# Performance work log

Hardware: AMD Instinct MI355X
Metric: run time of the kernel (lower is better)

The kernel has to match this reference:

```python
import jax, jax.numpy as jnp
import numpy as np

TAU = 1.0
TOP_P = 0.9
EPS = 1e-5


def _nucleus_adj(X, W1, W2, W3):
    h = jnp.tanh(X @ W1.T)            # [N, d_attn]
    q = h @ W2.T                      # [N, d_attn]
    k = X @ W3.T                      # [N, d_attn]
    scores = (q @ k.T) / TAU          # [N, N]
    probs = jax.nn.softmax(scores, axis=-1)
    # nucleus (top-p): keep smallest prefix of desc-sorted probs covering mass p
    order = jnp.argsort(-probs, axis=-1)
    sp = jnp.take_along_axis(probs, order, axis=-1)
    cs = jnp.cumsum(sp, axis=-1)
    keep_sorted = (cs - sp) < TOP_P   # keep tokens before mass exceeds p (incl. crossing one)
    inv = jnp.argsort(order, axis=-1)
    keep = jnp.take_along_axis(keep_sorted, inv, axis=-1)
    A = jnp.where(keep, probs, 0.0)
    return A / jnp.sum(A, axis=-1, keepdims=True)


def _sequence_priors(N, dtype):
    # forward/backward chain priors (S=None case): row-stochastic shift matrices
    Rf = jnp.eye(N, k=-1, dtype=dtype).at[0, 0].set(1.0)
    Rb = jnp.eye(N, k=1, dtype=dtype).at[N - 1, N - 1].set(1.0)
    return Rf, Rb


def setup_inputs() -> dict:
    key = jax.random.key(0)
    ks = jax.random.split(key, 8)
    N, d_in, d_attn, steps = 4096, 512, 64, 2
    s = 0.02
    return {
        "X": jax.random.normal(ks[0], (N, d_in), jnp.float32),
        "W1": jax.random.normal(ks[1], (d_attn, d_in), jnp.float32) * s,
        "W2": jax.random.normal(ks[2], (d_attn, d_attn), jnp.float32) * s,
        "W3": jax.random.normal(ks[3], (d_attn, d_in), jnp.float32) * s,
        "U1": jax.random.normal(ks[4], (steps, d_in, d_in), jnp.float32) * s,
        "U2": jax.random.normal(ks[5], (steps, d_in, d_in), jnp.float32) * s,
        "U3": jax.random.normal(ks[6], (steps, d_in, d_in), jnp.float32) * s,
        "gamma": jnp.ones((d_in,), jnp.float32),
        "beta": jnp.zeros((d_in,), jnp.float32),
    }


def reference(X, W1, W2, W3, U1, U2, U3, gamma, beta):
    N = X.shape[0]
    steps = U1.shape[0]
    Rf, Rb = _sequence_priors(N, X.dtype)
    Z = jnp.zeros_like(X)
    Xf, Xb, Xa = X, X, X
    for n in range(steps):
        A = _nucleus_adj(Xa, W1, W2, W3)
        Xf = Rf @ Xf
        Xb = Rb @ Xb
        Xa = A @ Xa
        P = Xf @ U1[n].T + Xb @ U2[n].T
        F = Xa @ U3[n].T
        Z = Z + (P + F)  # dropout is identity in eval mode
    y = X + Z
    mu = jnp.mean(y, axis=-1, keepdims=True)
    var = jnp.var(y, axis=-1, keepdims=True)
    return (y - mu) * jax.lax.rsqrt(var + EPS) * gamma + beta
```

## Files before the change

kernel.cpp:

```cpp
#include <hip/hip_runtime.h>
#include <hip/hip_bf16.h>
#include <math.h>

typedef short bf16x8 __attribute__((ext_vector_type(8)));
typedef float f32x4 __attribute__((ext_vector_type(4)));
typedef unsigned short u16;
typedef unsigned long long u64;

#define N_TOK  4096
#define D_IN   512
#define D_ATTN 64
#define NBI    1024
#define CAPW   128
#define TOPP   0.9f
#define LN_EPS 1e-5f
#define AMAXV  (N_TOK - 1)
#define FLTMAX 3.402823466e38f
#define MSCALE 524288.0f

__device__ __forceinline__ u16 f2bf(float f) {
  unsigned int u = __float_as_uint(f);
  return (u16)((u + 0x7FFFu + ((u >> 16) & 1u)) >> 16);
}

__device__ __forceinline__ float bf2f(u16 v) {
  return __uint_as_float(((unsigned)v) << 16);
}

__device__ __forceinline__ unsigned mfix(float e) {
  return (unsigned)(e * MSCALE + 0.5f);
}

__device__ __forceinline__ void gload16(const u16* g, u16* l) {
  __builtin_amdgcn_global_load_lds(
      (const __attribute__((address_space(1))) unsigned int*)g,
      (__attribute__((address_space(3))) unsigned int*)l, 16, 0, 0);
}

template<int EPI, int NSEG, int KSEG>
__global__ __launch_bounds__(256)
void gemm128(const u16* __restrict__ A0, int lda0, int sh0, const u16* __restrict__ B0, int ldb0,
             const u16* __restrict__ A1, int lda1, int sh1, const u16* __restrict__ B1, int ldb1,
             const u16* __restrict__ A2, int lda2, int sh2, const u16* __restrict__ B2, int ldb2,
             float* __restrict__ Cf, u16* __restrict__ Cb, u16* __restrict__ CbT,
             int ldc, int ldct)
{
  constexpr int BN = 64;
  constexpr int NF = BN / 32;
  __shared__ u16 sA[3][128 * 64];
  __shared__ u16 sB[3][BN * 64];

  const int tid  = threadIdx.x;
  const int wave = tid >> 6;
  const int lane = tid & 63;
  const int l15  = lane & 15;
  const int l4   = lane >> 4;
  const int brow = blockIdx.y << 7;
  const int bcol = blockIdx.x * BN;
  const int kz   = blockIdx.z * KSEG;
  const int wr64 = (wave >> 1) << 6;
  const int wcol = (wave & 1) * (BN >> 1);

  constexpr int IPSEG = KSEG >> 6;
  constexpr int TOTAL = NSEG * IPSEG;

  auto stage = [&](int buf, int it) {
    int seg = (NSEG == 1) ? 0 : (it / IPSEG);
    int kk  = (NSEG == 1) ? (it << 6) : ((it % IPSEG) << 6);
    const u16 *Ab, *Bb; int la, lb, sh;
    if (seg == 0)      { Ab = A0; la = lda0; sh = sh0; Bb = B0; lb = ldb0; }
    else if (seg == 1) { Ab = A1; la = lda1; sh = sh1; Bb = B1; lb = ldb1; }
    else               { Ab = A2; la = lda2; sh = sh2; Bb = B2; lb = ldb2; }
    kk += kz;
#pragma unroll
    for (int q = 0; q < 4; ++q) {
      int idx = q * 256 + tid;
      int row = idx >> 3;
      int chunk = (idx & 7) ^ (row & 7);
      int r = brow + row + sh;
      r = (r < 0) ? 0 : ((r > AMAXV) ? AMAXV : r);
      gload16(Ab + (size_t)r * la + kk + chunk * 8, &sA[buf][idx * 8]);
    }
#pragma unroll
    for (int q = 0; q < BN / 32; ++q) {
      int idx = q * 256 + tid;
      int row = idx >> 3;
      int chunk = (idx & 7) ^ (row & 7);
      gload16(Bb + (size_t)(bcol + row) * lb + kk + chunk * 8, &sB[buf][idx * 8]);
    }
  };

  f32x4 acc[4][NF];
#pragma unroll
  for (int m = 0; m < 4; ++m)
#pragma unroll
    for (int n = 0; n < NF; ++n) {
      acc[m][n][0] = 0.f; acc[m][n][1] = 0.f; acc[m][n][2] = 0.f; acc[m][n][3] = 0.f;
    }

  stage(0, 0);
  if (TOTAL > 1) stage(1, 1);

  for (int i = 0; i < TOTAL; ++i) {
    if (i + 1 < TOTAL) asm volatile("s_waitcnt vmcnt(6)" ::: "memory");
    else               asm volatile("s_waitcnt vmcnt(0)" ::: "memory");
    __builtin_amdgcn_s_barrier();
    if (i + 2 < TOTAL) stage((i + 2) % 3, i + 2);
    const int c = i % 3;
#pragma unroll
    for (int ks = 0; ks < 2; ++ks) {
      bf16x8 af[4], bfr[NF];
#pragma unroll
      for (int m = 0; m < 4; ++m) {
        int ar = wr64 + m * 16 + l15;
        af[m] = *(const bf16x8*)&sA[c][ar * 64 + (((ks << 2) + l4) ^ (ar & 7)) * 8];
      }
#pragma unroll
      for (int n = 0; n < NF; ++n) {
        int br = wcol + n * 16 + l15;
        bfr[n] = *(const bf16x8*)&sB[c][br * 64 + (((ks << 2) + l4) ^ (br & 7)) * 8];
      }
#pragma unroll
      for (int m = 0; m < 4; ++m)
#pragma unroll
        for (int n = 0; n < NF; ++n)
          acc[m][n] = __builtin_amdgcn_mfma_f32_16x16x32_bf16(af[m], bfr[n], acc[m][n], 0, 0, 0);
    }
  }

  float* Cf6 = (EPI == 6) ? (Cf + (size_t)blockIdx.z * (size_t)ldct) : Cf;
#pragma unroll
  for (int m = 0; m < 4; ++m)
#pragma unroll
    for (int n = 0; n < NF; ++n)
#pragma unroll
      for (int r = 0; r < 4; ++r) {
        const int row = brow + wr64 + m * 16 + l4 * 4 + r;
        const int col = bcol + wcol + n * 16 + l15;
        const float v = acc[m][n][r];
        if (EPI == 0) Cf[(size_t)row * ldc + col] = v;
        if (EPI == 1) Cb[(size_t)row * ldc + col] = f2bf(tanhf(v));
        if (EPI == 2) Cb[(size_t)row * ldc + col] = f2bf(v);
        if (EPI == 3) Cf[(size_t)row * ldc + col] += v;
        if (EPI == 4) {
          u16 hv = f2bf(v);
          Cb [(size_t)row * ldc  + col] = hv;
          CbT[(size_t)col * ldct + row] = hv;
        }
        if (EPI == 5) {
          if (col < 64) Cb [(size_t)row * 64 + col]        = f2bf(tanhf(v));
          else          CbT[(size_t)row * 64 + (col - 64)] = f2bf(v);
        }
        if (EPI == 6) Cf6[(size_t)row * ldc + col] = v;
      }
}

__global__ __launch_bounds__(256)
void pvfix(const float* __restrict__ Zp, u16* __restrict__ Xa, u16* __restrict__ XaT)
{
  const size_t st = (size_t)N_TOK * D_IN;
  __shared__ u16 tile[64][65];
  const int bx = blockIdx.x, by = blockIdx.y;
  const int t = threadIdx.x;
  const int tx = t & 15, ty = t >> 4;
#pragma unroll
  for (int i = 0; i < 4; ++i) {
    int r = by * 64 + ty + 16 * i;
    int c = bx * 64 + tx * 4;
    size_t idx = (size_t)r * D_IN + c;
    float4 a = *(const float4*)&Zp[idx];
    float4 b = *(const float4*)&Zp[idx + st];
    float4 d = *(const float4*)&Zp[idx + 2 * st];
    float4 e = *(const float4*)&Zp[idx + 3 * st];
    u16 q0 = f2bf(a.x + b.x + d.x + e.x), q1 = f2bf(a.y + b.y + d.y + e.y);
    u16 q2 = f2bf(a.z + b.z + d.z + e.z), q3 = f2bf(a.w + b.w + d.w + e.w);
    *(ushort4*)&Xa[idx] = make_ushort4(q0, q1, q2, q3);
    tile[ty + 16 * i][tx * 4 + 0] = q0;
    tile[ty + 16 * i][tx * 4 + 1] = q1;
    tile[ty + 16 * i][tx * 4 + 2] = q2;
    tile[ty + 16 * i][tx * 4 + 3] = q3;
  }
  __syncthreads();
#pragma unroll
  for (int i = 0; i < 4; ++i) {
    int cc = ty + 16 * i;
    int rq = tx * 4;
    u16 o0 = tile[rq + 0][cc], o1 = tile[rq + 1][cc];
    u16 o2 = tile[rq + 2][cc], o3 = tile[rq + 3][cc];
    *(ushort4*)&XaT[(size_t)(bx * 64 + cc) * N_TOK + by * 64 + rq] =
        make_ushort4(o0, o1, o2, o3);
  }
}

__global__ __launch_bounds__(256, 8)
void nucleus_block(const u16* __restrict__ S, u16* __restrict__ A, int apitch)
{
  const int t = threadIdx.x;
  const int wv = t >> 6, ln = t & 63;

  __shared__ unsigned hist[4][NBI];
  __shared__ float ge[CAPW];
  __shared__ unsigned gm[CAPW];
  __shared__ int   gcol[CAPW];
  __shared__ unsigned char kf[CAPW];
  __shared__ float sMax[4], sMin[4];
  __shared__ int   sCnt[4];
  __shared__ unsigned sScan[4];
  __shared__ u64   sKey[4];
  __shared__ int   s_cnt;

  for (int rr = 0; rr < 2; ++rr) {
    const int row = blockIdx.x + rr * (N_TOK / 2);
    const u16* srow = S + (size_t)row * N_TOK;
    u16* arow = A + (size_t)row * apitch;

    __syncthreads();

    float evf[16];
    float lmax = -FLTMAX, lmin = FLTMAX;
#pragma unroll
    for (int q = 0; q < 4; ++q) {
      ushort4 v = ((const ushort4*)srow)[q * 256 + t];
      float e0 = bf2f(v.x), e1 = bf2f(v.y), e2 = bf2f(v.z), e3 = bf2f(v.w);
      evf[4*q+0] = e0; evf[4*q+1] = e1; evf[4*q+2] = e2; evf[4*q+3] = e3;
      lmax = fmaxf(lmax, fmaxf(fmaxf(e0, e1), fmaxf(e2, e3)));
      lmin = fminf(lmin, fminf(fminf(e0, e1), fminf(e2, e3)));
    }
#pragma unroll
    for (int o = 32; o; o >>= 1) {
      lmax = fmaxf(lmax, __shfl_xor(lmax, o));
      lmin = fminf(lmin, __shfl_xor(lmin, o));
    }
    if (ln == 0) { sMax[wv] = lmax; sMin[wv] = lmin; }
    __syncthreads();
    const float smax = fmaxf(fmaxf(sMax[0], sMax[1]), fmaxf(sMax[2], sMax[3]));
    const float smin = fminf(fminf(sMin[0], sMin[1]), fminf(sMin[2], sMin[3]));

#pragma unroll
    for (int j = 0; j < 16; ++j) evf[j] = __expf(evf[j] - smax);

    unsigned keepM = 0, cand = 0xFFFFu;
    unsigned Agt = 0, T = 0;
    bool haveT = false;
    float lo = __expf(smin - smax);
    float width = fmaxf(1.0f - lo, 1e-30f);
    u64 denInt = 0;

    for (int lev = 0; lev < 12; ++lev) {
      if (lev > 0) {
        int myCnt = __popc(cand);
        float cmin = FLTMAX, cmax = -FLTMAX;
#pragma unroll
        for (int j = 0; j < 16; ++j)
          if ((cand >> j) & 1) { float e = evf[j]; cmin = fminf(cmin, e); cmax = fmaxf(cmax, e); }
        int ct = myCnt;
#pragma unroll
        for (int o = 32; o; o >>= 1) {
          ct   += __shfl_xor(ct, o);
          cmin  = fminf(cmin, __shfl_xor(cmin, o));
          cmax  = fmaxf(cmax, __shfl_xor(cmax, o));
        }
        if (ln == 0) { sCnt[wv] = ct; sMin[wv] = cmin; sMax[wv] = cmax; }
        __syncthreads();
        const int tot = sCnt[0] + sCnt[1] + sCnt[2] + sCnt[3];
        cmin = fminf(fminf(sMin[0], sMin[1]), fminf(sMin[2], sMin[3]));
        cmax = fmaxf(fmaxf(sMax[0], sMax[1]), fmaxf(sMax[2], sMax[3]));

        if (tot == 0) { denInt = Agt; break; }

        if (cmin == cmax || lev == 11) {
          const float v = cmax;
          const unsigned mv = mfix(v);
          int r;
          if (T <= Agt) r = 0;
          else if (mv == 0) r = tot;
          else { unsigned need = T - Agt; r = (int)((need + mv - 1) / mv); if (r > tot) r = tot; }
          int cq[4], excl[4];
#pragma unroll
          for (int q = 0; q < 4; ++q) {
            cq[q] = __popc((cand >> (4 * q)) & 0xF);
            int sc = cq[q];
#pragma unroll
            for (int o = 1; o < 64; o <<= 1) { int u = __shfl_up(sc, o); if (ln >= o) sc += u; }
            excl[q] = sc - cq[q];
            if (ln == 63) hist[wv][NBI - 4 + q] = (unsigned)(excl[q] + cq[q]);
          }
          __syncthreads();
          int qtot[4], woffq[4];
#pragma unroll
          for (int q = 0; q < 4; ++q) {
            unsigned w0 = hist[0][NBI - 4 + q], w1 = hist[1][NBI - 4 + q],
                     w2 = hist[2][NBI - 4 + q], w3 = hist[3][NBI - 4 + q];
            woffq[q] = (wv > 0 ? (int)w0 : 0) + (wv > 1 ? (int)w1 : 0) + (wv > 2 ? (int)w2 : 0);
            qtot[q]  = (int)(w0 + w1 + w2 + w3);
          }
          int qbase = 0;
#pragma unroll
          for (int q = 0; q < 4; ++q) {
            int seen = 0;
#pragma unroll
            for (int jj = 0; jj < 4; ++jj) {
              int j = 4 * q + jj;
              if ((cand >> j) & 1) {
                int rank = qbase + woffq[q] + excl[q] + seen;
                if (rank < r) keepM |= 1u << j;
                ++seen;
              }
            }
            qbase += qtot[q];
          }
          denInt = (u64)Agt + (u64)r * mv;
          break;
        }

        if (tot <= CAPW) {
          if (t == 0) s_cnt = 0;
          __syncthreads();
#pragma unroll
          for (int j = 0; j < 16; ++j) {
            if ((cand >> j) & 1) {
              int i = atomicAdd(&s_cnt, 1);
              ge[i] = evf[j];
              gm[i] = mfix(evf[j]);
              gcol[i] = ((j >> 2) << 10) + (t << 2) + (j & 3);
            }
          }
          __syncthreads();
          const int cnt = s_cnt;
          if (t < cnt) {
            float ei = ge[t]; int ci = gcol[t];
            unsigned m = Agt;
            for (int u = 0; u < cnt; ++u) {
              float el = ge[u];
              if (el > ei || (el == ei && gcol[u] < ci)) m += gm[u];
            }
            kf[t] = (m < T) ? 1 : 0;
          }
          __syncthreads();
          u64 ks = 0;
          for (int u = 0; u < cnt; ++u) {
            if (kf[u]) {
              ks += gm[u];
              int c = gcol[u];
              if (((c >> 2) & 255) == t)
                keepM |= 1u << (((c >> 10) << 2) | (c & 3));
            }
          }
          denInt = (u64)Agt + ks;
          break;
        }
      }

      const float scale = (float)NBI / width;
      {
        uint4 z; z.x = 0; z.y = 0; z.z = 0; z.w = 0;
        ((uint4*)hist[0])[t] = z; ((uint4*)hist[1])[t] = z;
        ((uint4*)hist[2])[t] = z; ((uint4*)hist[3])[t] = z;
      }
      __syncthreads();
      unsigned* Hw = hist[wv];
#pragma unroll
      for (int j = 0; j < 16; ++j) {
        if ((cand >> j) & 1) {
          float e = evf[j];
          int b = (int)((e - lo) * scale);
          b = (b < 0) ? 0 : ((b > NBI - 1) ? NBI - 1 : b);
          atomicAdd(&Hw[b], mfix(e));
        }
      }
      __syncthreads();
      unsigned hv[4];
      {
        uint4 a0 = ((const uint4*)hist[0])[t];
        uint4 a1 = ((const uint4*)hist[1])[t];
        uint4 a2 = ((const uint4*)hist[2])[t];
        uint4 a3 = ((const uint4*)hist[3])[t];
        hv[0] = a0.x + a1.x + a2.x + a3.x;
        hv[1] = a0.y + a1.y + a2.y + a3.y;
        hv[2] = a0.z + a1.z + a2.z + a3.z;
        hv[3] = a0.w + a1.w + a2.w + a3.w;
      }
      unsigned sl = (hv[0] + hv[1]) + (hv[2] + hv[3]);
      unsigned pv = sl;
#pragma unroll
      for (int o = 1; o < 64; o <<= 1) { unsigned u = __shfl_up(pv, o); if (ln >= o) pv += u; }
      if (ln == 63) sScan[wv] = pv;
      __syncthreads();
      const unsigned woff = (wv > 0 ? sScan[0] : 0u) + (wv > 1 ? sScan[1] : 0u) + (wv > 2 ? sScan[2] : 0u);
      const unsigned CM   = sScan[0] + sScan[1] + sScan[2] + sScan[3];
      if (!haveT) {
        T = (unsigned)((9ULL * (unsigned long long)CM) / 10ULL);
        haveT = true;
      }
      const unsigned incl = pv + woff;
      unsigned Arun = Agt + (CM - incl);
      int lb = -1; unsigned Ab = 0;
#pragma unroll
      for (int j = 3; j >= 0; --j) {
        unsigned bm = hv[j];
        if (Arun < T && Arun + bm >= T) { lb = j; Ab = Arun; }
        Arun += bm;
      }
      u64 key = (lb >= 0) ? (((u64)(unsigned)(((t << 2) | lb) + 1) << 32) | (u64)Ab) : 0ULL;
#pragma unroll
      for (int o = 32; o; o >>= 1) { u64 k2 = __shfl_xor(key, o); if (k2 > key) key = k2; }
      if (ln == 0) sKey[wv] = key;
      __syncthreads();
      u64 kmax = sKey[0];
      if (sKey[1] > kmax) kmax = sKey[1];
      if (sKey[2] > kmax) kmax = sKey[2];
      if (sKey[3] > kmax) kmax = sKey[3];
      const int s = (int)(unsigned)(kmax >> 32) - 1;
      if (s < 0) { keepM |= cand; denInt = (u64)Agt + CM; break; }
      const unsigned Abnd = (unsigned)kmax;
      unsigned nk = 0, nc = 0;
#pragma unroll
      for (int j = 0; j < 16; ++j) {
        if ((cand >> j) & 1) {
          float e = evf[j];
          int b = (int)((e - lo) * scale);
          b = (b < 0) ? 0 : ((b > NBI - 1) ? NBI - 1 : b);
          if (b > s) nk |= 1u << j;
          else if (b == s) nc |= 1u << j;
        }
      }
      keepM |= nk;
      cand = nc;
      Agt = Abnd;
      width = fmaxf(width * (1.0f / NBI), 1e-37f);
      lo = lo + (float)s * width;
    }

    float den = (float)denInt * (1.0f / MSCALE);
    if (denInt == 0) den = 1.f;
    const float invd = 1.0f / den;

#pragma unroll
    for (int q = 0; q < 4; ++q) {
      u16 rr4[4];
#pragma unroll
      for (int j = 0; j < 4; ++j) {
        int b = 4 * q + j;
        float val = ((keepM >> b) & 1) ? evf[b] * invd : 0.f;
        rr4[j] = f2bf(val);
      }
      ((ushort4*)arow)[q * 256 + t] = make_ushort4(rr4[0], rr4[1], rr4[2], rr4[3]);
    }
  }
}

__global__ void cvt_all(const float* __restrict__ X,  const float* __restrict__ W1,
                        const float* __restrict__ W3, const float* __restrict__ W2,
                        const float* __restrict__ U1, const float* __restrict__ U2,
                        const float* __restrict__ U3,
                        u16* __restrict__ Xbf, u16* __restrict__ Xa0,
                        u16* __restrict__ W13b, u16* __restrict__ W2b,
                        u16* __restrict__ U1b, u16* __restrict__ U2b, u16* __restrict__ U3b)
{
  const int NX = 524288, NW = 8192, NW2 = 1024, NU = 131072;
  const int TOT = NX + 2 * NW + NW2 + 3 * NU;
  const int stride = gridDim.x * 256;
  for (int i = blockIdx.x * 256 + threadIdx.x; i < TOT; i += stride) {
    const float* s; u16* d; int rel; bool dual = false;
    if (i < NX)                       { s = X;  d = Xbf;  rel = i; dual = true; }
    else if (i < NX + NW)             { s = W1; d = W13b; rel = i - NX; }
    else if (i < NX + 2*NW)           { s = W3; d = W13b + (size_t)4*NW; rel = i - NX - NW; }
    else if (i < NX + 2*NW + NW2)     { s = W2; d = W2b;  rel = i - NX - 2*NW; }
    else if (i < NX + 2*NW + NW2 + NU){ s = U1; d = U1b;  rel = i - NX - 2*NW - NW2; }
    else if (i < NX + 2*NW + NW2+2*NU){ s = U2; d = U2b;  rel = i - NX - 2*NW - NW2 - NU; }
    else                              { s = U3; d = U3b;  rel = i - NX - 2*NW - NW2 - 2*NU; }
    float4 v = ((const float4*)s)[rel];
    ushort4 o;
    o.x = f2bf(v.x); o.y = f2bf(v.y); o.z = f2bf(v.z); o.w = f2bf(v.w);
    ((ushort4*)d)[rel] = o;
    if (dual) ((ushort4*)Xa0)[rel] = o;
  }
}

__global__ __launch_bounds__(256)
void tpose_bf(const float* __restrict__ X, u16* __restrict__ XT)
{
  __shared__ u16 tile[32][33];
  const int bc = blockIdx.x * 32;
  const int br = blockIdx.y * 32;
  const int tx = threadIdx.x & 31, ty = threadIdx.x >> 5;
#pragma unroll
  for (int i = 0; i < 32; i += 8)
    tile[ty + i][tx] = f2bf(X[(size_t)(br + ty + i) * D_IN + bc + tx]);
  __syncthreads();
#pragma unroll
  for (int i = 0; i < 32; i += 8)
    XT[(size_t)(bc + ty + i) * N_TOK + br + tx] = tile[tx][ty + i];
}

__global__ __launch_bounds__(256)
void ln_kernel(const float* __restrict__ X, float* Z,
               const float* __restrict__ gamma, const float* __restrict__ beta)
{
  const int tid = threadIdx.x;
  __shared__ float red[4];
  __shared__ float s_mu, s_var;
  for (int rr = 0; rr < 2; ++rr) {
    const int row = blockIdx.x + rr * (N_TOK / 2);
    const size_t base = (size_t)row * D_IN;
    __syncthreads();
    float y0 = X[base + tid] + Z[base + tid];
    float y1 = X[base + tid + 256] + Z[base + tid + 256];
    float s = y0 + y1;
    for (int o = 32; o; o >>= 1) s += __shfl_xor(s, o);
    if ((tid & 63) == 0) red[tid >> 6] = s;
    __syncthreads();
    if (tid == 0) s_mu = (red[0] + red[1] + red[2] + red[3]) * (1.f / D_IN);
    __syncthreads();
    const float mu = s_mu;
    float d0 = y0 - mu, d1 = y1 - mu;
    float v = d0 * d0 + d1 * d1;
    for (int o = 32; o; o >>= 1) v += __shfl_xor(v, o);
    if ((tid & 63) == 0) red[tid >> 6] = v;
    __syncthreads();
    if (tid == 0) s_var = (red[0] + red[1] + red[2] + red[3]) * (1.f / D_IN);
    __syncthreads();
    const float rs = rsqrtf(s_var + LN_EPS);
    Z[base + tid]       = d0 * rs * gamma[tid]       + beta[tid];
    Z[base + tid + 256] = d1 * rs * gamma[tid + 256] + beta[tid + 256];
  }
}

extern "C" void kernel_launch(void* const* d_in, const int* in_sizes, int n_in,
                              void* d_out, int out_size, void* d_ws, size_t ws_size,
                              hipStream_t stream)
{
  const float* X     = (const float*)d_in[0];
  const float* W1    = (const float*)d_in[1];
  const float* W2    = (const float*)d_in[2];
  const float* W3    = (const float*)d_in[3];
  const float* U1    = (const float*)d_in[4];
  const float* U2    = (const float*)d_in[5];
  const float* U3    = (const float*)d_in[6];
  const float* gamma = (const float*)d_in[7];
  const float* beta  = (const float*)d_in[8];

  char* w = (char*)d_ws;
  u16* S16    = (u16*)w;              w += (size_t)N_TOK * N_TOK * 2;
  u16* Xbf    = (u16*)w;              w += (size_t)N_TOK * D_IN * 2;
  u16* Xa0    = (u16*)w;              w += (size_t)N_TOK * D_IN * 2;
  u16* Xa1    = (u16*)w;              w += (size_t)N_TOK * D_IN * 2;
  u16* XaT0   = (u16*)w;              w += (size_t)D_IN * N_TOK * 2;
  u16* XaT1   = (u16*)w;              w += (size_t)D_IN * N_TOK * 2;
  u16* hb     = (u16*)w;              w += (size_t)N_TOK * D_ATTN * 2;
  u16* qb     = (u16*)w;              w += (size_t)N_TOK * D_ATTN * 2;
  u16* kb     = (u16*)w;              w += (size_t)N_TOK * D_ATTN * 2;
  u16* W13b   = (u16*)w;              w += (size_t)2 * D_ATTN * D_IN * 2;
  u16* W2b    = (u16*)w;              w += (size_t)D_ATTN * D_ATTN * 2;
  u16* U1b    = (u16*)w;              w += (size_t)2 * D_IN * D_IN * 2;
  u16* U2b    = (u16*)w;              w += (size_t)2 * D_IN * D_IN * 2;
  u16* U3b    = (u16*)w;              w += (size_t)2 * D_IN * D_IN * 2;

  size_t used = (size_t)(w - (char*)d_ws);
  u16* Abuf;
  int  apitch = N_TOK;
  if (ws_size >= used + (size_t)N_TOK * N_TOK * 2) {
    Abuf = (u16*)w;
    w += (size_t)N_TOK * N_TOK * 2;
  } else {
    Abuf = S16;
  }
  used = (size_t)(w - (char*)d_ws);
  float* Zp = nullptr;
  const bool splitK = (ws_size >= used + 4 * (size_t)N_TOK * D_IN * 4);
  if (splitK) { Zp = (float*)w; w += 4 * (size_t)N_TOK * D_IN * 4; }

  float* Z = (float*)d_out;

  hipMemsetAsync(d_out, 0, (size_t)N_TOK * D_IN * 4, stream);

  cvt_all<<<1024, 256, 0, stream>>>(X, W1, W3, W2, U1, U2, U3,
                                    Xbf, Xa0, W13b, W2b, U1b, U2b, U3b);
  tpose_bf<<<dim3(D_IN / 32, N_TOK / 32), 256, 0, stream>>>(X, XaT0);

  u16* XaC[2]  = {Xa0, Xa1};
  u16* XaTC[2] = {XaT0, XaT1};

  for (int n = 0; n < 2; ++n) {
    const int cur = n & 1, nxt = cur ^ 1;
    const size_t uoff = (size_t)n * D_IN * D_IN;
    gemm128<5, 1, D_IN><<<dim3(2, 32), 256, 0, stream>>>(
        XaC[cur], D_IN, 0, W13b, D_IN,
        nullptr, 0, 0, nullptr, 0, nullptr, 0, 0, nullptr, 0,
        nullptr, hb, kb, 64, 64);
    gemm128<2, 1, D_ATTN><<<dim3(1, 32), 256, 0, stream>>>(
        hb, D_ATTN, 0, W2b, D_ATTN,
        nullptr, 0, 0, nullptr, 0, nullptr, 0, 0, nullptr, 0,
        nullptr, qb, nullptr, D_ATTN, 0);
    gemm128<2, 1, D_ATTN><<<dim3(64, 32), 256, 0, stream>>>(
        qb, D_ATTN, 0, kb, D_ATTN,
        nullptr, 0, 0, nullptr, 0, nullptr, 0, 0, nullptr, 0,
        nullptr, S16, nullptr, N_TOK, 0);
    nucleus_block<<<N_TOK / 2, 256, 0, stream>>>(S16, Abuf, apitch);
    if (splitK) {
      gemm128<6, 1, N_TOK / 4><<<dim3(8, 32, 4), 256, 0, stream>>>(
          Abuf, apitch, 0, XaTC[cur], N_TOK,
          nullptr, 0, 0, nullptr, 0, nullptr, 0, 0, nullptr, 0,
          Zp, nullptr, nullptr, D_IN, N_TOK * D_IN);
      pvfix<<<dim3(D_IN / 64, N_TOK / 64), 256, 0, stream>>>(
          Zp, XaC[nxt], XaTC[nxt]);
    } else {
      gemm128<4, 1, N_TOK><<<dim3(8, 32), 256, 0, stream>>>(
          Abuf, apitch, 0, XaTC[cur], N_TOK,
          nullptr, 0, 0, nullptr, 0, nullptr, 0, 0, nullptr, 0,
          nullptr, XaC[nxt], XaTC[nxt], D_IN, N_TOK);
    }
    gemm128<3, 3, D_IN><<<dim3(8, 32), 256, 0, stream>>>(
        Xbf, D_IN, -(n + 1), U1b + uoff, D_IN,
        Xbf, D_IN,  (n + 1), U2b + uoff, D_IN,
        XaC[nxt], D_IN, 0,   U3b + uoff, D_IN,
        Z, nullptr, nullptr, D_IN, 0);
  }

  ln_kernel<<<N_TOK / 2, 256, 0, stream>>>(X, Z, gamma, beta);
}
```

Before: 394.7 us.

## Split-K the projection GEMM over two slices and reduce in LayerNorm

The per-step projection GEMM (Xf·U1 + Xb·U2 + Xa·U3) now runs with a K-split of 2 into two separate fp32 accumulation buffers, which doubles the grid from 256 to 512 blocks. The final LayerNorm kernel sums both partial buffers. The GEMM's shared-memory triple buffer is sized to the iteration count, so short-K instantiations use less LDS. The occupancy hint on nucleus_block is also removed. The cost is an extra 16 MB zero-fill and extra partial-sum traffic in exchange for better occupancy of the projection GEMM.

```diff
diff --git a/kernel.cpp b/kernel.cpp
--- a/kernel.cpp
+++ b/kernel.cpp
@@ -47,8 +47,12 @@
 {
   constexpr int BN = 64;
   constexpr int NF = BN / 32;
-  __shared__ u16 sA[3][128 * 64];
-  __shared__ u16 sB[3][BN * 64];
+  constexpr int IPSEG = KSEG >> 6;
+  constexpr int TOTAL = NSEG * IPSEG;
+  constexpr int DB = (TOTAL < 3) ? TOTAL : 3;
+
+  __shared__ u16 sA[DB][128 * 64];
+  __shared__ u16 sB[DB][BN * 64];
 
   const int tid  = threadIdx.x;
   const int wave = tid >> 6;
@@ -61,9 +65,6 @@
   const int wr64 = (wave >> 1) << 6;
   const int wcol = (wave & 1) * (BN >> 1);
 
-  constexpr int IPSEG = KSEG >> 6;
-  constexpr int TOTAL = NSEG * IPSEG;
-
   auto stage = [&](int buf, int it) {
     int seg = (NSEG == 1) ? 0 : (it / IPSEG);
     int kk  = (NSEG == 1) ? (it << 6) : ((it % IPSEG) << 6);
@@ -99,14 +100,14 @@
     }
 
   stage(0, 0);
-  if (TOTAL > 1) stage(1, 1);
+  if (TOTAL > 1) stage(1 % DB, 1);
 
   for (int i = 0; i < TOTAL; ++i) {
     if (i + 1 < TOTAL) asm volatile("s_waitcnt vmcnt(6)" ::: "memory");
     else               asm volatile("s_waitcnt vmcnt(0)" ::: "memory");
     __builtin_amdgcn_s_barrier();
-    if (i + 2 < TOTAL) stage((i + 2) % 3, i + 2);
-    const int c = i % 3;
+    if (i + 2 < TOTAL) stage((i + 2) % DB, i + 2);
+    const int c = i % DB;
 #pragma unroll
     for (int ks = 0; ks < 2; ++ks) {
       bf16x8 af[4], bfr[NF];
@@ -128,7 +129,7 @@
     }
   }
 
-  float* Cf6 = (EPI == 6) ? (Cf + (size_t)blockIdx.z * (size_t)ldct) : Cf;
+  float* Cfz = (EPI == 6 || EPI == 3) ? (Cf + (size_t)blockIdx.z * (size_t)ldct) : Cf;
 #pragma unroll
   for (int m = 0; m < 4; ++m)
 #pragma unroll
@@ -141,7 +142,7 @@
         if (EPI == 0) Cf[(size_t)row * ldc + col] = v;
         if (EPI == 1) Cb[(size_t)row * ldc + col] = f2bf(tanhf(v));
         if (EPI == 2) Cb[(size_t)row * ldc + col] = f2bf(v);
-        if (EPI == 3) Cf[(size_t)row * ldc + col] += v;
+        if (EPI == 3) Cfz[(size_t)row * ldc + col] += v;
         if (EPI == 4) {
           u16 hv = f2bf(v);
           Cb [(size_t)row * ldc  + col] = hv;
@@ -151,7 +152,7 @@
           if (col < 64) Cb [(size_t)row * 64 + col]        = f2bf(tanhf(v));
           else          CbT[(size_t)row * 64 + (col - 64)] = f2bf(v);
         }
-        if (EPI == 6) Cf6[(size_t)row * ldc + col] = v;
+        if (EPI == 6) Cfz[(size_t)row * ldc + col] = v;
       }
 }
 
@@ -192,7 +193,7 @@
   }
 }
 
-__global__ __launch_bounds__(256, 8)
+__global__ __launch_bounds__(256)
 void nucleus_block(const u16* __restrict__ S, u16* __restrict__ A, int apitch)
 {
   const int t = threadIdx.x;
@@ -494,7 +495,8 @@
 }
 
 __global__ __launch_bounds__(256)
-void ln_kernel(const float* __restrict__ X, float* Z,
+void ln_kernel(const float* __restrict__ X, const float* __restrict__ Z0,
+               const float* __restrict__ Z1, float* __restrict__ OUT,
                const float* __restrict__ gamma, const float* __restrict__ beta)
 {
   const int tid = threadIdx.x;
@@ -504,8 +506,9 @@
     const int row = blockIdx.x + rr * (N_TOK / 2);
     const size_t base = (size_t)row * D_IN;
     __syncthreads();
-    float y0 = X[base + tid] + Z[base + tid];
-    float y1 = X[base + tid + 256] + Z[base + tid + 256];
+    float y0 = X[base + tid] + Z0[base + tid];
+    float y1 = X[base + tid + 256] + Z0[base + tid + 256];
+    if (Z1) { y0 += Z1[base + tid]; y1 += Z1[base + tid + 256]; }
     float s = y0 + y1;
     for (int o = 32; o; o >>= 1) s += __shfl_xor(s, o);
     if ((tid & 63) == 0) red[tid >> 6] = s;
@@ -521,8 +524,8 @@
     if (tid == 0) s_var = (red[0] + red[1] + red[2] + red[3]) * (1.f / D_IN);
     __syncthreads();
     const float rs = rsqrtf(s_var + LN_EPS);
-    Z[base + tid]       = d0 * rs * gamma[tid]       + beta[tid];
-    Z[base + tid + 256] = d1 * rs * gamma[tid + 256] + beta[tid + 256];
+    OUT[base + tid]       = d0 * rs * gamma[tid]       + beta[tid];
+    OUT[base + tid + 256] = d1 * rs * gamma[tid + 256] + beta[tid + 256];
   }
 }
 
@@ -569,10 +572,18 @@
   float* Zp = nullptr;
   const bool splitK = (ws_size >= used + 4 * (size_t)N_TOK * D_IN * 4);
   if (splitK) { Zp = (float*)w; w += 4 * (size_t)N_TOK * D_IN * 4; }
+  used = (size_t)(w - (char*)d_ws);
+  float* Zq = nullptr;
+  const bool projSplit = (ws_size >= used + 2 * (size_t)N_TOK * D_IN * 4);
+  if (projSplit) { Zq = (float*)w; w += 2 * (size_t)N_TOK * D_IN * 4; }
 
   float* Z = (float*)d_out;
 
-  hipMemsetAsync(d_out, 0, (size_t)N_TOK * D_IN * 4, stream);
+  if (projSplit) {
+    hipMemsetAsync(Zq, 0, 2 * (size_t)N_TOK * D_IN * 4, stream);
+  } else {
+    hipMemsetAsync(d_out, 0, (size_t)N_TOK * D_IN * 4, stream);
+  }
 
   cvt_all<<<1024, 256, 0, stream>>>(X, W1, W3, W2, U1, U2, U3,
                                     Xbf, Xa0, W13b, W2b, U1b, U2b, U3b);
@@ -610,12 +621,26 @@
           nullptr, 0, 0, nullptr, 0, nullptr, 0, 0, nullptr, 0,
           nullptr, XaC[nxt], XaTC[nxt], D_IN, N_TOK);
     }
-    gemm128<3, 3, D_IN><<<dim3(8, 32), 256, 0, stream>>>(
-        Xbf, D_IN, -(n + 1), U1b + uoff, D_IN,
-        Xbf, D_IN,  (n + 1), U2b + uoff, D_IN,
-        XaC[nxt], D_IN, 0,   U3b + uoff, D_IN,
-        Z, nullptr, nullptr, D_IN, 0);
-  }
-
-  ln_kernel<<<N_TOK / 2, 256, 0, stream>>>(X, Z, gamma, beta);
-}
+    if (projSplit) {
+      gemm128<3, 3, D_IN / 2><<<dim3(8, 32, 2), 256, 0, stream>>>(
+          Xbf, D_IN, -(n + 1), U1b + uoff, D_IN,
+          Xbf, D_IN,  (n + 1), U2b + uoff, D_IN,
+          XaC[nxt], D_IN, 0,   U3b + uoff, D_IN,
+          Zq, nullptr, nullptr, D_IN, N_TOK * D_IN);
+    } else {
+      gemm128<3, 3, D_IN><<<dim3(8, 32), 256, 0, stream>>>(
+          Xbf, D_IN, -(n + 1), U1b + uoff, D_IN,
+          Xbf, D_IN,  (n + 1), U2b + uoff, D_IN,
+          XaC[nxt], D_IN, 0,   U3b + uoff, D_IN,
+          Z, nullptr, nullptr, D_IN, 0);
+    }
+  }
+
+  if (projSplit) {
+    ln_kernel<<<N_TOK / 2, 256, 0, stream>>>(
+        X, Zq, Zq + (size_t)N_TOK * D_IN, (float*)d_out, gamma, beta);
+  } else {
+    ln_kernel<<<N_TOK / 2, 256, 0, stream>>>(
+        X, Z, nullptr, (float*)d_out, gamma, beta);
+  }
+}
```

After: 346.0 us. 1.14x faster.
